# Kernel optimization log

Hardware: AMD Instinct MI355X
Metric: run time of the kernel (lower is better)

The kernel has to match this reference:

```python
import jax, jax.numpy as jnp
import numpy as np

N = 4096
IN_F = 512
OUT_F = 64
N_HEADS = 8
ALPHA = 0.2
NEG_INF = -9e15


def setup_inputs() -> dict:
    key = jax.random.key(0)
    k1, k2, k3, k4 = jax.random.split(key, 4)
    h = jax.random.normal(k1, (N, IN_F), dtype=jnp.float32)
    adj = jax.random.randint(k2, (N, N), 0, 2, dtype=jnp.int32)
    W = jax.random.normal(k3, (IN_F, OUT_F * N_HEADS), dtype=jnp.float32) * (1.414 / np.sqrt(IN_F))
    a = jax.random.normal(k4, (2 * OUT_F, 1), dtype=jnp.float32) * 0.1
    return {"h": h, "adj": adj, "W": W, "a": a}


def reference(h, adj, W, a):
    # Wh: [N, H, F]
    Wh = (h @ W).reshape(N, N_HEADS, OUT_F)
    # The all-pairs concat + matmul with a ([2F,1], shared across heads)
    # decomposes exactly: e[i,j,h] = leakyrelu(Wh[i,h]@a[:F] + Wh[j,h]@a[F:])
    a_src = a[:OUT_F, 0]
    a_dst = a[OUT_F:, 0]
    src = jnp.einsum('nhf,f->nh', Wh, a_src)  # [N, H]
    dst = jnp.einsum('nhf,f->nh', Wh, a_dst)  # [N, H]
    e = src[:, None, :] + dst[None, :, :]      # [N, N, H]
    e = jnp.where(e > 0, e, ALPHA * e)         # leaky relu
    e = jnp.where(adj[:, :, None] > 0, e, NEG_INF)
    attention = jax.nn.softmax(e, axis=1)      # softmax over neighbors j
    h_prime = jnp.einsum('ijh,jhf->ihf', attention, Wh)  # [N, H, F]
    out = h_prime.reshape(N, N_HEADS * OUT_F)
    return jax.nn.elu(out)
```

## Files before the change

### kernel.cpp

```cpp
#include <hip/hip_runtime.h>
#include <hip/hip_bf16.h>


typedef unsigned short ushort_t;
typedef __attribute__((ext_vector_type(8))) short bf16x8;
typedef __attribute__((ext_vector_type(4))) float f32x4;

#define LOG2E 1.4426950408889634f

__device__ __forceinline__ ushort_t f2bf(float x) {
    unsigned u = __builtin_bit_cast(unsigned, x);
    u += 0x7FFFu + ((u >> 16) & 1u);
    return (ushort_t)(u >> 16);
}

__global__ __launch_bounds__(256) void transpose_w(const float* __restrict__ W,
                                                   ushort_t* __restrict__ WT) {
    __shared__ ushort_t t[32][33];
    int bx = blockIdx.x & 15, by = blockIdx.x >> 4;
    int tx = threadIdx.x & 31, ty = threadIdx.x >> 5;
#pragma unroll
    for (int i = 0; i < 32; i += 8)
        t[ty + i][tx] = f2bf(W[(by * 32 + ty + i) * 512 + bx * 32 + tx]);
    __syncthreads();
#pragma unroll
    for (int i = 0; i < 32; i += 8)
        WT[(bx * 32 + ty + i) * 512 + by * 32 + tx] = t[tx][ty + i];
}

__global__ __launch_bounds__(256) void gemm_whT(const ushort_t* __restrict__ WT,
                                                const float* __restrict__ h,
                                                const float* __restrict__ a,
                                                ushort_t* __restrict__ WhT,
                                                float* __restrict__ srcv,
                                                float* __restrict__ dstv) {
    __shared__ ushort_t Al[64][40];
    __shared__ ushort_t Bl[64][40];
    __shared__ float asrc[64], adst[64];
    __shared__ float sred[2][4][64];
    int tid = threadIdx.x;
    int wave = tid >> 6, lane = tid & 63, quad = lane >> 4, nn = lane & 15;
    int mb = blockIdx.x & 7, nb = blockIdx.x >> 3;
    if (tid < 64) {
        asrc[tid] = a[tid] * LOG2E;
        adst[tid] = a[64 + tid] * LOG2E;
    }
    int r = tid >> 2, part = tid & 3;
    const ushort_t* Ag = WT + (long)(mb * 64 + r) * 512 + part * 8;
    const float* Bg = h + (long)(nb * 64 + r) * 512 + part * 8;
    f32x4 acc[4] = {};
    for (int kb = 0; kb < 512; kb += 32) {
        __syncthreads();
        *(bf16x8*)&Al[r][part * 8] = *(const bf16x8*)(Ag + kb);
        float4 f0 = *(const float4*)(Bg + kb);
        float4 f1 = *(const float4*)(Bg + kb + 4);
        bf16x8 bvv;
        bvv[0] = (short)f2bf(f0.x); bvv[1] = (short)f2bf(f0.y);
        bvv[2] = (short)f2bf(f0.z); bvv[3] = (short)f2bf(f0.w);
        bvv[4] = (short)f2bf(f1.x); bvv[5] = (short)f2bf(f1.y);
        bvv[6] = (short)f2bf(f1.z); bvv[7] = (short)f2bf(f1.w);
        *(bf16x8*)&Bl[r][part * 8] = bvv;
        __syncthreads();
        bf16x8 af = *(const bf16x8*)&Al[wave * 16 + nn][quad * 8];
#pragma unroll
        for (int nt = 0; nt < 4; nt++) {
            bf16x8 bv = *(const bf16x8*)&Bl[nt * 16 + nn][quad * 8];
            acc[nt] = __builtin_amdgcn_mfma_f32_16x16x32_bf16(af, bv, acc[nt], 0, 0, 0);
        }
    }
    int row0 = mb * 64 + wave * 16 + quad * 4;
    int col0 = nb * 64 + nn;
    int f0i = wave * 16 + quad * 4;
#pragma unroll
    for (int nt = 0; nt < 4; nt++) {
        float s = 0.f, d = 0.f;
#pragma unroll
        for (int rr = 0; rr < 4; rr++) {
            float v = acc[nt][rr];
            WhT[(long)(row0 + rr) * 4096 + col0 + nt * 16] = f2bf(v);
            s += v * asrc[f0i + rr];
            d += v * adst[f0i + rr];
        }
        s += __shfl_xor(s, 16); s += __shfl_xor(s, 32);
        d += __shfl_xor(d, 16); d += __shfl_xor(d, 32);
        if (quad == 0) { sred[0][wave][nt * 16 + nn] = s; sred[1][wave][nt * 16 + nn] = d; }
    }
    __syncthreads();
    if (tid < 64)
        srcv[(long)mb * 4096 + nb * 64 + tid] =
            sred[0][0][tid] + sred[0][1][tid] + sred[0][2][tid] + sred[0][3][tid];
    else if (tid < 128) {
        int c = tid - 64;
        dstv[(long)mb * 4096 + nb * 64 + c] =
            sred[1][0][c] + sred[1][1][c] + sred[1][2][c] + sred[1][3][c];
    }
}

__global__ __launch_bounds__(512, 4) void gat_attn(const int* __restrict__ adj,
                                                   const ushort_t* __restrict__ WhT,
                                                   const float* __restrict__ srcv,
                                                   const float* __restrict__ dstv,
                                                   float* __restrict__ out) {
    __shared__ __align__(16) ushort_t Vb[2][128][72];
    __shared__ __align__(16) ushort_t Pb[2][2][32][72];
    __shared__ float denoml[2][32];
    int tid = threadIdx.x;
    int wave = tid >> 6, lane = tid & 63, quad = lane >> 4, nn = lane & 15;
    int hb = blockIdx.x >> 7, ib = blockIdx.x & 127;
    int i0 = ib * 32;
    int hh = tid >> 8, tt = tid & 255;
    int pi = tt >> 3, jo = tt & 7;
    int head = hb * 2 + hh;
    float srcV = srcv[(long)head * 4096 + i0 + pi];
    const int* adjP = adj + (long)(i0 + pi) * 4096 + jo * 8;
    const float* dstP = dstv + (long)head * 4096 + jo * 8;
    int vr = tid >> 3, vcs = tid & 7;
    const ushort_t* Vg0 = WhT + (long)(hb * 128 + vr) * 4096 + vcs * 8;
    const ushort_t* Vg1 = WhT + (long)(hb * 128 + 64 + vr) * 4096 + vcs * 8;
    int jhalf = wave >> 2, ws = wave & 3;
    int strip = ws & 1, whead = ws >> 1;

    int4 pa[2][2]; float4 pd[2][2]; bf16x8 pvv[2][2];
    {
        pa[0][0] = *(const int4*)(adjP);
        pa[0][1] = *(const int4*)(adjP + 4);
        pd[0][0] = *(const float4*)(dstP);
        pd[0][1] = *(const float4*)(dstP + 4);
        pvv[0][0] = *(const bf16x8*)(Vg0);
        pvv[0][1] = *(const bf16x8*)(Vg1);
    }
    f32x4 acc[4] = {};
    float dpart = 0.f;
#pragma unroll 2
    for (int k = 0; k < 64; k++) {
        int cb = k & 1;
        if (k < 63) {
            long jb = (long)(k + 1) * 64;
            pa[cb ^ 1][0] = *(const int4*)(adjP + jb);
            pa[cb ^ 1][1] = *(const int4*)(adjP + jb + 4);
            pd[cb ^ 1][0] = *(const float4*)(dstP + jb);
            pd[cb ^ 1][1] = *(const float4*)(dstP + jb + 4);
            pvv[cb ^ 1][0] = *(const bf16x8*)(Vg0 + jb);
            pvv[cb ^ 1][1] = *(const bf16x8*)(Vg1 + jb);
        }
        bf16x8 pv;
        float wsum = 0.f;
#pragma unroll
        for (int q = 0; q < 2; q++) {
            int4 av = pa[cb][q];
            float4 dv = pd[cb][q];
            float e, ww;
            e = srcV + dv.x; e = fmaxf(e, 0.2f * e);
            ww = __builtin_amdgcn_exp2f(av.x > 0 ? e : -10000.f);
            wsum += ww; pv[q * 4 + 0] = (short)f2bf(ww);
            e = srcV + dv.y; e = fmaxf(e, 0.2f * e);
            ww = __builtin_amdgcn_exp2f(av.y > 0 ? e : -10000.f);
            wsum += ww; pv[q * 4 + 1] = (short)f2bf(ww);
            e = srcV + dv.z; e = fmaxf(e, 0.2f * e);
            ww = __builtin_amdgcn_exp2f(av.z > 0 ? e : -10000.f);
            wsum += ww; pv[q * 4 + 2] = (short)f2bf(ww);
            e = srcV + dv.w; e = fmaxf(e, 0.2f * e);
            ww = __builtin_amdgcn_exp2f(av.w > 0 ? e : -10000.f);
            wsum += ww; pv[q * 4 + 3] = (short)f2bf(ww);
        }
        dpart += wsum;
        *(bf16x8*)&Pb[cb][hh][pi][jo * 8] = pv;
        *(bf16x8*)&Vb[cb][vr][vcs * 8] = pvv[cb][0];
        *(bf16x8*)&Vb[cb][64 + vr][vcs * 8] = pvv[cb][1];
        if (k > 0) {
            int pb = cb ^ 1;
            bf16x8 af = *(const bf16x8*)&Pb[pb][whead][strip * 16 + nn][jhalf * 32 + quad * 8];
#pragma unroll
            for (int nt = 0; nt < 4; nt++) {
                bf16x8 bv = *(const bf16x8*)&Vb[pb][whead * 64 + nt * 16 + nn][jhalf * 32 + quad * 8];
                acc[nt] = __builtin_amdgcn_mfma_f32_16x16x32_bf16(af, bv, acc[nt], 0, 0, 0);
            }
        }
        __syncthreads();
    }
    {
        bf16x8 af = *(const bf16x8*)&Pb[1][whead][strip * 16 + nn][jhalf * 32 + quad * 8];
#pragma unroll
        for (int nt = 0; nt < 4; nt++) {
            bf16x8 bv = *(const bf16x8*)&Vb[1][whead * 64 + nt * 16 + nn][jhalf * 32 + quad * 8];
            acc[nt] = __builtin_amdgcn_mfma_f32_16x16x32_bf16(af, bv, acc[nt], 0, 0, 0);
        }
    }
    float dsum = dpart;
    dsum += __shfl_xor(dsum, 1);
    dsum += __shfl_xor(dsum, 2);
    dsum += __shfl_xor(dsum, 4);
    if ((tid & 7) == 0) denoml[hh][pi] = dsum;
    __syncthreads();
    float (*cmb)[64][20] = reinterpret_cast<float (*)[64][20]>(&Vb[0][0][0]);
    if (jhalf == 1) {
#pragma unroll
        for (int nt = 0; nt < 4; nt++)
            *(f32x4*)&cmb[ws][lane][nt * 4] = acc[nt];
    }
    __syncthreads();
    if (jhalf == 0) {
#pragma unroll
        for (int nt = 0; nt < 4; nt++) {
            f32x4 o = acc[nt] + *(const f32x4*)&cmb[ws][lane][nt * 4];
#pragma unroll
            for (int rr = 0; rr < 4; rr++) {
                int il = strip * 16 + quad * 4 + rr;
                float d = fmaxf(denoml[whead][il], 1e-30f);
                float v = o[rr] / d;
                v = v > 0.f ? v : __expf(v) - 1.f;
                out[(long)(i0 + il) * 512 + hb * 128 + whead * 64 + nt * 16 + nn] = v;
            }
        }
    }
}

extern "C" void kernel_launch(void* const* d_in, const int* in_sizes, int n_in,
                              void* d_out, int out_size, void* d_ws, size_t ws_size,
                              hipStream_t stream) {
    const float* h   = (const float*)d_in[0];
    const int*   adj = (const int*)d_in[1];
    const float* W   = (const float*)d_in[2];
    const float* a   = (const float*)d_in[3];

    char* ws = (char*)d_ws;
    ushort_t* WhT = (ushort_t*)ws;
    ushort_t* WT  = (ushort_t*)(ws + (4u << 20));
    float* srcv   = (float*)(ws + (4u << 20) + (512u << 10));
    float* dstv   = srcv + 8 * 4096;

    transpose_w<<<256, 256, 0, stream>>>(W, WT);
    gemm_whT<<<512, 256, 0, stream>>>(WT, h, a, WhT, srcv, dstv);
    gat_attn<<<512, 512, 0, stream>>>(adj, WhT, srcv, dstv, (float*)d_out);
}
```

Baseline: 197.2 us.

## Factor attention exponentials into per-node products and read V straight from global

Precomputes exp2 of the source and destination scores (plain and 0.2-scaled) per node, so each attention weight becomes a compare, select and multiply instead of an exp per edge. The weight is truncated to bf16 by bit masking and packing. The attention kernel now uses 16-row tiles with 1024 blocks and an occupancy hint of 8, and loads WhT fragments directly from global memory instead of staging them through LDS. The projection GEMM also drops its LDS staging and reads operands directly. Risks are overflow or underflow of the factored exponentials with no max subtraction, truncation instead of rounding to bf16, and more global traffic for V.

```diff
diff --git a/kernel.cpp b/kernel.cpp
--- a/kernel.cpp
+++ b/kernel.cpp
@@ -32,10 +32,11 @@
                                                 const float* __restrict__ h,
                                                 const float* __restrict__ a,
                                                 ushort_t* __restrict__ WhT,
-                                                float* __restrict__ srcv,
-                                                float* __restrict__ dstv) {
-    __shared__ ushort_t Al[64][40];
-    __shared__ ushort_t Bl[64][40];
+                                                float* __restrict__ expA,
+                                                float* __restrict__ expC,
+                                                float* __restrict__ expT,
+                                                float* __restrict__ expB,
+                                                float* __restrict__ expD) {
     __shared__ float asrc[64], adst[64];
     __shared__ float sred[2][4][64];
     int tid = threadIdx.x;
@@ -45,29 +46,26 @@
         asrc[tid] = a[tid] * LOG2E;
         adst[tid] = a[64 + tid] * LOG2E;
     }
-    int r = tid >> 2, part = tid & 3;
-    const ushort_t* Ag = WT + (long)(mb * 64 + r) * 512 + part * 8;
-    const float* Bg = h + (long)(nb * 64 + r) * 512 + part * 8;
+    const ushort_t* Ap = WT + (unsigned)((mb * 64 + wave * 16 + nn) * 512 + quad * 8);
+    const float* Hb = h + (unsigned)((nb * 64 + nn) * 512 + quad * 8);
     f32x4 acc[4] = {};
+#pragma unroll 4
     for (int kb = 0; kb < 512; kb += 32) {
-        __syncthreads();
-        *(bf16x8*)&Al[r][part * 8] = *(const bf16x8*)(Ag + kb);
-        float4 f0 = *(const float4*)(Bg + kb);
-        float4 f1 = *(const float4*)(Bg + kb + 4);
-        bf16x8 bvv;
-        bvv[0] = (short)f2bf(f0.x); bvv[1] = (short)f2bf(f0.y);
-        bvv[2] = (short)f2bf(f0.z); bvv[3] = (short)f2bf(f0.w);
-        bvv[4] = (short)f2bf(f1.x); bvv[5] = (short)f2bf(f1.y);
-        bvv[6] = (short)f2bf(f1.z); bvv[7] = (short)f2bf(f1.w);
-        *(bf16x8*)&Bl[r][part * 8] = bvv;
-        __syncthreads();
-        bf16x8 af = *(const bf16x8*)&Al[wave * 16 + nn][quad * 8];
+        bf16x8 af = *(const bf16x8*)(Ap + kb);
 #pragma unroll
         for (int nt = 0; nt < 4; nt++) {
-            bf16x8 bv = *(const bf16x8*)&Bl[nt * 16 + nn][quad * 8];
+            const float* hp = Hb + nt * 16 * 512 + kb;
+            float4 f0 = *(const float4*)hp;
+            float4 f1 = *(const float4*)(hp + 4);
+            bf16x8 bv;
+            bv[0] = (short)f2bf(f0.x); bv[1] = (short)f2bf(f0.y);
+            bv[2] = (short)f2bf(f0.z); bv[3] = (short)f2bf(f0.w);
+            bv[4] = (short)f2bf(f1.x); bv[5] = (short)f2bf(f1.y);
+            bv[6] = (short)f2bf(f1.z); bv[7] = (short)f2bf(f1.w);
             acc[nt] = __builtin_amdgcn_mfma_f32_16x16x32_bf16(af, bv, acc[nt], 0, 0, 0);
         }
     }
+    __syncthreads();
     int row0 = mb * 64 + wave * 16 + quad * 4;
     int col0 = nb * 64 + nn;
     int f0i = wave * 16 + quad * 4;
@@ -77,7 +75,7 @@
 #pragma unroll
         for (int rr = 0; rr < 4; rr++) {
             float v = acc[nt][rr];
-            WhT[(long)(row0 + rr) * 4096 + col0 + nt * 16] = f2bf(v);
+            WhT[(unsigned)((row0 + rr) * 4096 + col0 + nt * 16)] = f2bf(v);
             s += v * asrc[f0i + rr];
             d += v * adst[f0i + rr];
         }
@@ -86,131 +84,118 @@
         if (quad == 0) { sred[0][wave][nt * 16 + nn] = s; sred[1][wave][nt * 16 + nn] = d; }
     }
     __syncthreads();
-    if (tid < 64)
-        srcv[(long)mb * 4096 + nb * 64 + tid] =
-            sred[0][0][tid] + sred[0][1][tid] + sred[0][2][tid] + sred[0][3][tid];
-    else if (tid < 128) {
+    if (tid < 64) {
+        float s = sred[0][0][tid] + sred[0][1][tid] + sred[0][2][tid] + sred[0][3][tid];
+        unsigned idx = mb * 4096 + nb * 64 + tid;
+        expA[idx] = __builtin_amdgcn_exp2f(s);
+        expC[idx] = __builtin_amdgcn_exp2f(0.2f * s);
+        expT[idx] = __builtin_amdgcn_exp2f(-s);
+    } else if (tid < 128) {
         int c = tid - 64;
-        dstv[(long)mb * 4096 + nb * 64 + c] =
-            sred[1][0][c] + sred[1][1][c] + sred[1][2][c] + sred[1][3][c];
-    }
-}
-
-__global__ __launch_bounds__(512, 4) void gat_attn(const int* __restrict__ adj,
+        float d = sred[1][0][c] + sred[1][1][c] + sred[1][2][c] + sred[1][3][c];
+        unsigned idx = mb * 4096 + nb * 64 + c;
+        expB[idx] = __builtin_amdgcn_exp2f(d);
+        expD[idx] = __builtin_amdgcn_exp2f(0.2f * d);
+    }
+}
+
+__global__ __launch_bounds__(512, 8) void gat_attn(const int* __restrict__ adj,
                                                    const ushort_t* __restrict__ WhT,
-                                                   const float* __restrict__ srcv,
-                                                   const float* __restrict__ dstv,
+                                                   const float* __restrict__ expA,
+                                                   const float* __restrict__ expC,
+                                                   const float* __restrict__ expT,
+                                                   const float* __restrict__ expB,
+                                                   const float* __restrict__ expD,
                                                    float* __restrict__ out) {
-    __shared__ __align__(16) ushort_t Vb[2][128][72];
-    __shared__ __align__(16) ushort_t Pb[2][2][32][72];
-    __shared__ float denoml[2][32];
+    __shared__ __align__(16) ushort_t Pb[2][2][16][72];
+    __shared__ float denoml[2][16];
+    __shared__ __align__(16) float cmb[2][2][64][8];
     int tid = threadIdx.x;
     int wave = tid >> 6, lane = tid & 63, quad = lane >> 4, nn = lane & 15;
-    int hb = blockIdx.x >> 7, ib = blockIdx.x & 127;
-    int i0 = ib * 32;
+    int hb = blockIdx.x & 3, ib = blockIdx.x >> 2;
+    int i0 = ib * 16;
     int hh = tid >> 8, tt = tid & 255;
-    int pi = tt >> 3, jo = tt & 7;
+    int pi = tt >> 4, jo = tt & 15;
     int head = hb * 2 + hh;
-    float srcV = srcv[(long)head * 4096 + i0 + pi];
-    const int* adjP = adj + (long)(i0 + pi) * 4096 + jo * 8;
-    const float* dstP = dstv + (long)head * 4096 + jo * 8;
-    int vr = tid >> 3, vcs = tid & 7;
-    const ushort_t* Vg0 = WhT + (long)(hb * 128 + vr) * 4096 + vcs * 8;
-    const ushort_t* Vg1 = WhT + (long)(hb * 128 + 64 + vr) * 4096 + vcs * 8;
-    int jhalf = wave >> 2, ws = wave & 3;
-    int strip = ws & 1, whead = ws >> 1;
-
-    int4 pa[2][2]; float4 pd[2][2]; bf16x8 pvv[2][2];
-    {
-        pa[0][0] = *(const int4*)(adjP);
-        pa[0][1] = *(const int4*)(adjP + 4);
-        pd[0][0] = *(const float4*)(dstP);
-        pd[0][1] = *(const float4*)(dstP + 4);
-        pvv[0][0] = *(const bf16x8*)(Vg0);
-        pvv[0][1] = *(const bf16x8*)(Vg1);
-    }
-    f32x4 acc[4] = {};
+    float Ai = expA[head * 4096 + i0 + pi];
+    float Ci = expC[head * 4096 + i0 + pi];
+    float Ti = expT[head * 4096 + i0 + pi];
+    unsigned aoff = (unsigned)(i0 + pi) * 4096 + jo * 4;
+    unsigned boff = (unsigned)head * 4096 + jo * 4;
+    int whead = wave & 1, jhalf = (wave >> 1) & 1, nhalf = wave >> 2;
+    unsigned voff0 = (unsigned)(hb * 128 + whead * 64 + nhalf * 32 + nn) * 4096
+                     + jhalf * 32 + quad * 8;
+    unsigned voff1 = voff0 + 16u * 4096u;
+    f32x4 acc0 = {}, acc1 = {};
     float dpart = 0.f;
+    int4 pa = *(const int4*)(adj + aoff);
 #pragma unroll 2
     for (int k = 0; k < 64; k++) {
         int cb = k & 1;
-        if (k < 63) {
-            long jb = (long)(k + 1) * 64;
-            pa[cb ^ 1][0] = *(const int4*)(adjP + jb);
-            pa[cb ^ 1][1] = *(const int4*)(adjP + jb + 4);
-            pd[cb ^ 1][0] = *(const float4*)(dstP + jb);
-            pd[cb ^ 1][1] = *(const float4*)(dstP + jb + 4);
-            pvv[cb ^ 1][0] = *(const bf16x8*)(Vg0 + jb);
-            pvv[cb ^ 1][1] = *(const bf16x8*)(Vg1 + jb);
-        }
-        bf16x8 pv;
-        float wsum = 0.f;
-#pragma unroll
-        for (int q = 0; q < 2; q++) {
-            int4 av = pa[cb][q];
-            float4 dv = pd[cb][q];
-            float e, ww;
-            e = srcV + dv.x; e = fmaxf(e, 0.2f * e);
-            ww = __builtin_amdgcn_exp2f(av.x > 0 ? e : -10000.f);
-            wsum += ww; pv[q * 4 + 0] = (short)f2bf(ww);
-            e = srcV + dv.y; e = fmaxf(e, 0.2f * e);
-            ww = __builtin_amdgcn_exp2f(av.y > 0 ? e : -10000.f);
-            wsum += ww; pv[q * 4 + 1] = (short)f2bf(ww);
-            e = srcV + dv.z; e = fmaxf(e, 0.2f * e);
-            ww = __builtin_amdgcn_exp2f(av.z > 0 ? e : -10000.f);
-            wsum += ww; pv[q * 4 + 2] = (short)f2bf(ww);
-            e = srcV + dv.w; e = fmaxf(e, 0.2f * e);
-            ww = __builtin_amdgcn_exp2f(av.w > 0 ? e : -10000.f);
-            wsum += ww; pv[q * 4 + 3] = (short)f2bf(ww);
-        }
-        dpart += wsum;
-        *(bf16x8*)&Pb[cb][hh][pi][jo * 8] = pv;
-        *(bf16x8*)&Vb[cb][vr][vcs * 8] = pvv[cb][0];
-        *(bf16x8*)&Vb[cb][64 + vr][vcs * 8] = pvv[cb][1];
+        int4 av = pa;
+        if (k < 63) pa = *(const int4*)(adj + aoff + (k + 1) * 64);
+        float4 Bv = *(const float4*)(expB + boff + k * 64);
+        float4 Dv = *(const float4*)(expD + boff + k * 64);
+        unsigned w0, w1, w2, w3;
+        {
+            float s1, s2, w;
+            s1 = Bv.x > Ti ? Bv.x : Dv.x;  s2 = Bv.x > Ti ? Ai : Ci;  w = s1 * s2;
+            w0 = __builtin_bit_cast(unsigned, w) & 0xFFFF0000u;  w0 = av.x > 0 ? w0 : 0u;
+            s1 = Bv.y > Ti ? Bv.y : Dv.y;  s2 = Bv.y > Ti ? Ai : Ci;  w = s1 * s2;
+            w1 = __builtin_bit_cast(unsigned, w) & 0xFFFF0000u;  w1 = av.y > 0 ? w1 : 0u;
+            s1 = Bv.z > Ti ? Bv.z : Dv.z;  s2 = Bv.z > Ti ? Ai : Ci;  w = s1 * s2;
+            w2 = __builtin_bit_cast(unsigned, w) & 0xFFFF0000u;  w2 = av.z > 0 ? w2 : 0u;
+            s1 = Bv.w > Ti ? Bv.w : Dv.w;  s2 = Bv.w > Ti ? Ai : Ci;  w = s1 * s2;
+            w3 = __builtin_bit_cast(unsigned, w) & 0xFFFF0000u;  w3 = av.w > 0 ? w3 : 0u;
+        }
+        dpart += __builtin_bit_cast(float, w0) + __builtin_bit_cast(float, w1)
+               + __builtin_bit_cast(float, w2) + __builtin_bit_cast(float, w3);
+        unsigned q0 = __builtin_amdgcn_perm(w1, w0, 0x07060302u);
+        unsigned q1 = __builtin_amdgcn_perm(w3, w2, 0x07060302u);
+        *(uint2*)&Pb[cb][hh][pi][jo * 4] = make_uint2(q0, q1);
         if (k > 0) {
-            int pb = cb ^ 1;
-            bf16x8 af = *(const bf16x8*)&Pb[pb][whead][strip * 16 + nn][jhalf * 32 + quad * 8];
-#pragma unroll
-            for (int nt = 0; nt < 4; nt++) {
-                bf16x8 bv = *(const bf16x8*)&Vb[pb][whead * 64 + nt * 16 + nn][jhalf * 32 + quad * 8];
-                acc[nt] = __builtin_amdgcn_mfma_f32_16x16x32_bf16(af, bv, acc[nt], 0, 0, 0);
-            }
+            int pbuf = cb ^ 1;
+            bf16x8 af = *(const bf16x8*)&Pb[pbuf][whead][nn][jhalf * 32 + quad * 8];
+            bf16x8 b0 = *(const bf16x8*)(WhT + voff0 + (k - 1) * 64);
+            bf16x8 b1 = *(const bf16x8*)(WhT + voff1 + (k - 1) * 64);
+            acc0 = __builtin_amdgcn_mfma_f32_16x16x32_bf16(af, b0, acc0, 0, 0, 0);
+            acc1 = __builtin_amdgcn_mfma_f32_16x16x32_bf16(af, b1, acc1, 0, 0, 0);
         }
         __syncthreads();
     }
     {
-        bf16x8 af = *(const bf16x8*)&Pb[1][whead][strip * 16 + nn][jhalf * 32 + quad * 8];
-#pragma unroll
-        for (int nt = 0; nt < 4; nt++) {
-            bf16x8 bv = *(const bf16x8*)&Vb[1][whead * 64 + nt * 16 + nn][jhalf * 32 + quad * 8];
-            acc[nt] = __builtin_amdgcn_mfma_f32_16x16x32_bf16(af, bv, acc[nt], 0, 0, 0);
-        }
+        bf16x8 af = *(const bf16x8*)&Pb[1][whead][nn][jhalf * 32 + quad * 8];
+        bf16x8 b0 = *(const bf16x8*)(WhT + voff0 + 63 * 64);
+        bf16x8 b1 = *(const bf16x8*)(WhT + voff1 + 63 * 64);
+        acc0 = __builtin_amdgcn_mfma_f32_16x16x32_bf16(af, b0, acc0, 0, 0, 0);
+        acc1 = __builtin_amdgcn_mfma_f32_16x16x32_bf16(af, b1, acc1, 0, 0, 0);
     }
     float dsum = dpart;
     dsum += __shfl_xor(dsum, 1);
     dsum += __shfl_xor(dsum, 2);
     dsum += __shfl_xor(dsum, 4);
-    if ((tid & 7) == 0) denoml[hh][pi] = dsum;
-    __syncthreads();
-    float (*cmb)[64][20] = reinterpret_cast<float (*)[64][20]>(&Vb[0][0][0]);
+    dsum += __shfl_xor(dsum, 8);
+    if ((lane & 15) == 0) denoml[hh][pi] = dsum;
     if (jhalf == 1) {
-#pragma unroll
-        for (int nt = 0; nt < 4; nt++)
-            *(f32x4*)&cmb[ws][lane][nt * 4] = acc[nt];
+        *(f32x4*)&cmb[whead][nhalf][lane][0] = acc0;
+        *(f32x4*)&cmb[whead][nhalf][lane][4] = acc1;
     }
     __syncthreads();
     if (jhalf == 0) {
-#pragma unroll
-        for (int nt = 0; nt < 4; nt++) {
-            f32x4 o = acc[nt] + *(const f32x4*)&cmb[ws][lane][nt * 4];
-#pragma unroll
-            for (int rr = 0; rr < 4; rr++) {
-                int il = strip * 16 + quad * 4 + rr;
-                float d = fmaxf(denoml[whead][il], 1e-30f);
-                float v = o[rr] / d;
-                v = v > 0.f ? v : __expf(v) - 1.f;
-                out[(long)(i0 + il) * 512 + hb * 128 + whead * 64 + nt * 16 + nn] = v;
-            }
+        f32x4 o0 = acc0 + *(const f32x4*)&cmb[whead][nhalf][lane][0];
+        f32x4 o1 = acc1 + *(const f32x4*)&cmb[whead][nhalf][lane][4];
+#pragma unroll
+        for (int rr = 0; rr < 4; rr++) {
+            int il = quad * 4 + rr;
+            float dnm = fmaxf(denoml[whead][il], 1e-30f);
+            float v0 = o0[rr] / dnm;
+            float v1 = o1[rr] / dnm;
+            v0 = v0 > 0.f ? v0 : __expf(v0) - 1.f;
+            v1 = v1 > 0.f ? v1 : __expf(v1) - 1.f;
+            unsigned oi = (unsigned)(i0 + il) * 512 + hb * 128 + whead * 64
+                        + nhalf * 32 + nn;
+            out[oi] = v0;
+            out[oi + 16] = v1;
         }
     }
 }
@@ -226,10 +211,14 @@
     char* ws = (char*)d_ws;
     ushort_t* WhT = (ushort_t*)ws;
     ushort_t* WT  = (ushort_t*)(ws + (4u << 20));
-    float* srcv   = (float*)(ws + (4u << 20) + (512u << 10));
-    float* dstv   = srcv + 8 * 4096;
+    float* expA = (float*)(ws + (4u << 20) + (512u << 10));
+    float* expC = expA + 8 * 4096;
+    float* expT = expC + 8 * 4096;
+    float* expB = expT + 8 * 4096;
+    float* expD = expB + 8 * 4096;
 
     transpose_w<<<256, 256, 0, stream>>>(W, WT);
-    gemm_whT<<<512, 256, 0, stream>>>(WT, h, a, WhT, srcv, dstv);
-    gat_attn<<<512, 512, 0, stream>>>(adj, WhT, srcv, dstv, (float*)d_out);
-}
+    gemm_whT<<<512, 256, 0, stream>>>(WT, h, a, WhT, expA, expC, expT, expB, expD);
+    gat_attn<<<1024, 512, 0, stream>>>(adj, WhT, expA, expC, expT, expB, expD,
+                                       (float*)d_out);
+}
```

New measurement: 290.4 us. +47.2%, slower.

## Factor softmax exponent into precomputed per-node exp terms, drop per-pair exp2

Applied to the files above, without the earlier changes.

Applies the identity exp2(leakyrelu(s+d)) = max(2^s·2^d, 2^(0.2s)·2^(0.2d)) and precomputes the four per-node exponentials in the GEMM epilogue. The attention inner loop then needs only multiplies, a max, truncation to bf16 by masking, and a byte permute, with no per-pair transcendental. The dst-vector loads move from register prefetch to in-loop loads, and the epilogue combine is split into two passes so it fits a smaller shared buffer. Risks: no max subtraction, so 2^s can overflow for large logits, bf16 conversion becomes truncation instead of round-to-nearest, and addressing switches to 32-bit unsigned.

```diff
diff --git a/kernel.cpp b/kernel.cpp
--- a/kernel.cpp
+++ b/kernel.cpp
@@ -32,8 +32,10 @@
                                                 const float* __restrict__ h,
                                                 const float* __restrict__ a,
                                                 ushort_t* __restrict__ WhT,
-                                                float* __restrict__ srcv,
-                                                float* __restrict__ dstv) {
+                                                float* __restrict__ expA,
+                                                float* __restrict__ expC,
+                                                float* __restrict__ expB,
+                                                float* __restrict__ expD) {
     __shared__ ushort_t Al[64][40];
     __shared__ ushort_t Bl[64][40];
     __shared__ float asrc[64], adst[64];
@@ -46,8 +48,8 @@
         adst[tid] = a[64 + tid] * LOG2E;
     }
     int r = tid >> 2, part = tid & 3;
-    const ushort_t* Ag = WT + (long)(mb * 64 + r) * 512 + part * 8;
-    const float* Bg = h + (long)(nb * 64 + r) * 512 + part * 8;
+    const ushort_t* Ag = WT + (unsigned)((mb * 64 + r) * 512 + part * 8);
+    const float* Bg = h + (unsigned)((nb * 64 + r) * 512 + part * 8);
     f32x4 acc[4] = {};
     for (int kb = 0; kb < 512; kb += 32) {
         __syncthreads();
@@ -77,7 +79,7 @@
 #pragma unroll
         for (int rr = 0; rr < 4; rr++) {
             float v = acc[nt][rr];
-            WhT[(long)(row0 + rr) * 4096 + col0 + nt * 16] = f2bf(v);
+            WhT[(unsigned)((row0 + rr) * 4096 + col0 + nt * 16)] = f2bf(v);
             s += v * asrc[f0i + rr];
             d += v * adst[f0i + rr];
         }
@@ -86,20 +88,26 @@
         if (quad == 0) { sred[0][wave][nt * 16 + nn] = s; sred[1][wave][nt * 16 + nn] = d; }
     }
     __syncthreads();
-    if (tid < 64)
-        srcv[(long)mb * 4096 + nb * 64 + tid] =
-            sred[0][0][tid] + sred[0][1][tid] + sred[0][2][tid] + sred[0][3][tid];
-    else if (tid < 128) {
+    if (tid < 64) {
+        float s = sred[0][0][tid] + sred[0][1][tid] + sred[0][2][tid] + sred[0][3][tid];
+        unsigned idx = mb * 4096 + nb * 64 + tid;
+        expA[idx] = __builtin_amdgcn_exp2f(s);
+        expC[idx] = __builtin_amdgcn_exp2f(0.2f * s);
+    } else if (tid < 128) {
         int c = tid - 64;
-        dstv[(long)mb * 4096 + nb * 64 + c] =
-            sred[1][0][c] + sred[1][1][c] + sred[1][2][c] + sred[1][3][c];
+        float d = sred[1][0][c] + sred[1][1][c] + sred[1][2][c] + sred[1][3][c];
+        unsigned idx = mb * 4096 + nb * 64 + c;
+        expB[idx] = __builtin_amdgcn_exp2f(d);
+        expD[idx] = __builtin_amdgcn_exp2f(0.2f * d);
     }
 }
 
 __global__ __launch_bounds__(512, 4) void gat_attn(const int* __restrict__ adj,
                                                    const ushort_t* __restrict__ WhT,
-                                                   const float* __restrict__ srcv,
-                                                   const float* __restrict__ dstv,
+                                                   const float* __restrict__ expA,
+                                                   const float* __restrict__ expC,
+                                                   const float* __restrict__ expB,
+                                                   const float* __restrict__ expD,
                                                    float* __restrict__ out) {
     __shared__ __align__(16) ushort_t Vb[2][128][72];
     __shared__ __align__(16) ushort_t Pb[2][2][32][72];
@@ -111,68 +119,76 @@
     int hh = tid >> 8, tt = tid & 255;
     int pi = tt >> 3, jo = tt & 7;
     int head = hb * 2 + hh;
-    float srcV = srcv[(long)head * 4096 + i0 + pi];
-    const int* adjP = adj + (long)(i0 + pi) * 4096 + jo * 8;
-    const float* dstP = dstv + (long)head * 4096 + jo * 8;
+    float Ai = expA[head * 4096 + i0 + pi];
+    float Ci = expC[head * 4096 + i0 + pi];
+    const int* adjP = adj + (unsigned)(i0 + pi) * 4096 + jo * 8;
+    const float* Bp = expB + (unsigned)head * 4096 + jo * 8;
+    const float* Dp = expD + (unsigned)head * 4096 + jo * 8;
     int vr = tid >> 3, vcs = tid & 7;
-    const ushort_t* Vg0 = WhT + (long)(hb * 128 + vr) * 4096 + vcs * 8;
-    const ushort_t* Vg1 = WhT + (long)(hb * 128 + 64 + vr) * 4096 + vcs * 8;
+    const ushort_t* Vg0 = WhT + (unsigned)(hb * 128 + vr) * 4096 + vcs * 8;
+    const ushort_t* Vg1 = Vg0 + 64u * 4096u;
     int jhalf = wave >> 2, ws = wave & 3;
     int strip = ws & 1, whead = ws >> 1;
-
-    int4 pa[2][2]; float4 pd[2][2]; bf16x8 pvv[2][2];
-    {
-        pa[0][0] = *(const int4*)(adjP);
-        pa[0][1] = *(const int4*)(adjP + 4);
-        pd[0][0] = *(const float4*)(dstP);
-        pd[0][1] = *(const float4*)(dstP + 4);
-        pvv[0][0] = *(const bf16x8*)(Vg0);
-        pvv[0][1] = *(const bf16x8*)(Vg1);
-    }
     f32x4 acc[4] = {};
     float dpart = 0.f;
+    int4 pa[2][2]; bf16x8 pvv[2][2];
+    pa[0][0] = *(const int4*)(adjP);
+    pa[0][1] = *(const int4*)(adjP + 4);
+    pvv[0][0] = *(const bf16x8*)(Vg0);
+    pvv[0][1] = *(const bf16x8*)(Vg1);
 #pragma unroll 2
     for (int k = 0; k < 64; k++) {
         int cb = k & 1;
-        if (k < 63) {
-            long jb = (long)(k + 1) * 64;
-            pa[cb ^ 1][0] = *(const int4*)(adjP + jb);
-            pa[cb ^ 1][1] = *(const int4*)(adjP + jb + 4);
-            pd[cb ^ 1][0] = *(const float4*)(dstP + jb);
-            pd[cb ^ 1][1] = *(const float4*)(dstP + jb + 4);
-            pvv[cb ^ 1][0] = *(const bf16x8*)(Vg0 + jb);
-            pvv[cb ^ 1][1] = *(const bf16x8*)(Vg1 + jb);
-        }
-        bf16x8 pv;
-        float wsum = 0.f;
-#pragma unroll
-        for (int q = 0; q < 2; q++) {
-            int4 av = pa[cb][q];
-            float4 dv = pd[cb][q];
-            float e, ww;
-            e = srcV + dv.x; e = fmaxf(e, 0.2f * e);
-            ww = __builtin_amdgcn_exp2f(av.x > 0 ? e : -10000.f);
-            wsum += ww; pv[q * 4 + 0] = (short)f2bf(ww);
-            e = srcV + dv.y; e = fmaxf(e, 0.2f * e);
-            ww = __builtin_amdgcn_exp2f(av.y > 0 ? e : -10000.f);
-            wsum += ww; pv[q * 4 + 1] = (short)f2bf(ww);
-            e = srcV + dv.z; e = fmaxf(e, 0.2f * e);
-            ww = __builtin_amdgcn_exp2f(av.z > 0 ? e : -10000.f);
-            wsum += ww; pv[q * 4 + 2] = (short)f2bf(ww);
-            e = srcV + dv.w; e = fmaxf(e, 0.2f * e);
-            ww = __builtin_amdgcn_exp2f(av.w > 0 ? e : -10000.f);
-            wsum += ww; pv[q * 4 + 3] = (short)f2bf(ww);
-        }
-        dpart += wsum;
-        *(bf16x8*)&Pb[cb][hh][pi][jo * 8] = pv;
+        float4 Bv0 = *(const float4*)(Bp + k * 64);
+        float4 Bv1 = *(const float4*)(Bp + k * 64 + 4);
+        float4 Dv0 = *(const float4*)(Dp + k * 64);
+        float4 Dv1 = *(const float4*)(Dp + k * 64 + 4);
+        int4 a0 = pa[cb][0], a1 = pa[cb][1];
+        unsigned w0, w1, w2, w3, w4, w5, w6, w7;
+        {
+            float w;
+            w = fmaxf(Ai * Bv0.x, Ci * Dv0.x);
+            w0 = __builtin_bit_cast(unsigned, w) & 0xFFFF0000u;  w0 = a0.x > 0 ? w0 : 0u;
+            w = fmaxf(Ai * Bv0.y, Ci * Dv0.y);
+            w1 = __builtin_bit_cast(unsigned, w) & 0xFFFF0000u;  w1 = a0.y > 0 ? w1 : 0u;
+            w = fmaxf(Ai * Bv0.z, Ci * Dv0.z);
+            w2 = __builtin_bit_cast(unsigned, w) & 0xFFFF0000u;  w2 = a0.z > 0 ? w2 : 0u;
+            w = fmaxf(Ai * Bv0.w, Ci * Dv0.w);
+            w3 = __builtin_bit_cast(unsigned, w) & 0xFFFF0000u;  w3 = a0.w > 0 ? w3 : 0u;
+            w = fmaxf(Ai * Bv1.x, Ci * Dv1.x);
+            w4 = __builtin_bit_cast(unsigned, w) & 0xFFFF0000u;  w4 = a1.x > 0 ? w4 : 0u;
+            w = fmaxf(Ai * Bv1.y, Ci * Dv1.y);
+            w5 = __builtin_bit_cast(unsigned, w) & 0xFFFF0000u;  w5 = a1.y > 0 ? w5 : 0u;
+            w = fmaxf(Ai * Bv1.z, Ci * Dv1.z);
+            w6 = __builtin_bit_cast(unsigned, w) & 0xFFFF0000u;  w6 = a1.z > 0 ? w6 : 0u;
+            w = fmaxf(Ai * Bv1.w, Ci * Dv1.w);
+            w7 = __builtin_bit_cast(unsigned, w) & 0xFFFF0000u;  w7 = a1.w > 0 ? w7 : 0u;
+        }
+        dpart += __builtin_bit_cast(float, w0) + __builtin_bit_cast(float, w1)
+               + __builtin_bit_cast(float, w2) + __builtin_bit_cast(float, w3)
+               + __builtin_bit_cast(float, w4) + __builtin_bit_cast(float, w5)
+               + __builtin_bit_cast(float, w6) + __builtin_bit_cast(float, w7);
+        uint4 pq;
+        pq.x = __builtin_amdgcn_perm(w1, w0, 0x07060302u);
+        pq.y = __builtin_amdgcn_perm(w3, w2, 0x07060302u);
+        pq.z = __builtin_amdgcn_perm(w5, w4, 0x07060302u);
+        pq.w = __builtin_amdgcn_perm(w7, w6, 0x07060302u);
+        *(uint4*)&Pb[cb][hh][pi][jo * 8] = pq;
         *(bf16x8*)&Vb[cb][vr][vcs * 8] = pvv[cb][0];
         *(bf16x8*)&Vb[cb][64 + vr][vcs * 8] = pvv[cb][1];
+        if (k < 63) {
+            const int* ap = adjP + (k + 1) * 64;
+            pa[cb ^ 1][0] = *(const int4*)(ap);
+            pa[cb ^ 1][1] = *(const int4*)(ap + 4);
+            pvv[cb ^ 1][0] = *(const bf16x8*)(Vg0 + (k + 1) * 64);
+            pvv[cb ^ 1][1] = *(const bf16x8*)(Vg1 + (k + 1) * 64);
+        }
         if (k > 0) {
-            int pb = cb ^ 1;
-            bf16x8 af = *(const bf16x8*)&Pb[pb][whead][strip * 16 + nn][jhalf * 32 + quad * 8];
+            int pbuf = cb ^ 1;
+            bf16x8 af = *(const bf16x8*)&Pb[pbuf][whead][strip * 16 + nn][jhalf * 32 + quad * 8];
 #pragma unroll
             for (int nt = 0; nt < 4; nt++) {
-                bf16x8 bv = *(const bf16x8*)&Vb[pb][whead * 64 + nt * 16 + nn][jhalf * 32 + quad * 8];
+                bf16x8 bv = *(const bf16x8*)&Vb[pbuf][whead * 64 + nt * 16 + nn][jhalf * 32 + quad * 8];
                 acc[nt] = __builtin_amdgcn_mfma_f32_16x16x32_bf16(af, bv, acc[nt], 0, 0, 0);
             }
         }
@@ -192,25 +208,48 @@
     dsum += __shfl_xor(dsum, 4);
     if ((tid & 7) == 0) denoml[hh][pi] = dsum;
     __syncthreads();
-    float (*cmb)[64][20] = reinterpret_cast<float (*)[64][20]>(&Vb[0][0][0]);
+    float (*cmb)[64][8] = reinterpret_cast<float (*)[64][8]>(&Vb[0][0][0]);
     if (jhalf == 1) {
-#pragma unroll
-        for (int nt = 0; nt < 4; nt++)
-            *(f32x4*)&cmb[ws][lane][nt * 4] = acc[nt];
+        *(f32x4*)&cmb[ws][lane][0] = acc[0] ;
+        *(f32x4*)&cmb[ws][lane][4] = acc[1];
     }
     __syncthreads();
     if (jhalf == 0) {
-#pragma unroll
-        for (int nt = 0; nt < 4; nt++) {
-            f32x4 o = acc[nt] + *(const f32x4*)&cmb[ws][lane][nt * 4];
-#pragma unroll
-            for (int rr = 0; rr < 4; rr++) {
-                int il = strip * 16 + quad * 4 + rr;
-                float d = fmaxf(denoml[whead][il], 1e-30f);
-                float v = o[rr] / d;
-                v = v > 0.f ? v : __expf(v) - 1.f;
-                out[(long)(i0 + il) * 512 + hb * 128 + whead * 64 + nt * 16 + nn] = v;
-            }
+        f32x4 o0 = acc[0] + *(const f32x4*)&cmb[ws][lane][0];
+        f32x4 o1 = acc[1] + *(const f32x4*)&cmb[ws][lane][4];
+#pragma unroll
+        for (int rr = 0; rr < 4; rr++) {
+            int il = strip * 16 + quad * 4 + rr;
+            float dnm = fmaxf(denoml[whead][il], 1e-30f);
+            float v0 = o0[rr] / dnm;
+            float v1 = o1[rr] / dnm;
+            v0 = v0 > 0.f ? v0 : __expf(v0) - 1.f;
+            v1 = v1 > 0.f ? v1 : __expf(v1) - 1.f;
+            unsigned oi = (unsigned)(i0 + il) * 512 + hb * 128 + whead * 64 + nn;
+            out[oi] = v0;
+            out[oi + 16] = v1;
+        }
+    }
+    __syncthreads();
+    if (jhalf == 1) {
+        *(f32x4*)&cmb[ws][lane][0] = acc[2];
+        *(f32x4*)&cmb[ws][lane][4] = acc[3];
+    }
+    __syncthreads();
+    if (jhalf == 0) {
+        f32x4 o0 = acc[2] + *(const f32x4*)&cmb[ws][lane][0];
+        f32x4 o1 = acc[3] + *(const f32x4*)&cmb[ws][lane][4];
+#pragma unroll
+        for (int rr = 0; rr < 4; rr++) {
+            int il = strip * 16 + quad * 4 + rr;
+            float dnm = fmaxf(denoml[whead][il], 1e-30f);
+            float v0 = o0[rr] / dnm;
+            float v1 = o1[rr] / dnm;
+            v0 = v0 > 0.f ? v0 : __expf(v0) - 1.f;
+            v1 = v1 > 0.f ? v1 : __expf(v1) - 1.f;
+            unsigned oi = (unsigned)(i0 + il) * 512 + hb * 128 + whead * 64 + 32 + nn;
+            out[oi] = v0;
+            out[oi + 16] = v1;
         }
     }
 }
@@ -226,10 +265,13 @@
     char* ws = (char*)d_ws;
     ushort_t* WhT = (ushort_t*)ws;
     ushort_t* WT  = (ushort_t*)(ws + (4u << 20));
-    float* srcv   = (float*)(ws + (4u << 20) + (512u << 10));
-    float* dstv   = srcv + 8 * 4096;
+    float* expA = (float*)(ws + (4u << 20) + (512u << 10));
+    float* expC = expA + 8 * 4096;
+    float* expB = expC + 8 * 4096;
+    float* expD = expB + 8 * 4096;
 
     transpose_w<<<256, 256, 0, stream>>>(W, WT);
-    gemm_whT<<<512, 256, 0, stream>>>(WT, h, a, WhT, srcv, dstv);
-    gat_attn<<<512, 512, 0, stream>>>(adj, WhT, srcv, dstv, (float*)d_out);
-}
+    gemm_whT<<<512, 256, 0, stream>>>(WT, h, a, WhT, expA, expC, expB, expD);
+    gat_attn<<<512, 512, 0, stream>>>(adj, WhT, expA, expC, expB, expD,
+                                      (float*)d_out);
+}
```

Result: no change. 200.7 us (+1.7%).
